# Kernel optimization log

Measured on AMD Instinct MI355X. Metric: run time of the kernel, lower is better.

The kernel has to match this reference:

```python
import jax, jax.numpy as jnp
import numpy as np

N, R, E, H, F = 50000, 6, 32768, 256, 16
NH, HD = 8, 32
EPS_LN = 1e-5

def _ln(x, g, b):
    mu = x.mean(-1, keepdims=True)
    var = ((x - mu) ** 2).mean(-1, keepdims=True)
    return (x - mu) * jax.lax.rsqrt(var + EPS_LN) * g + b

def setup_inputs() -> dict:
    key = jax.random.key(0)
    ks = jax.random.split(key, 32)
    s = lambda i, shape, scale=0.05: jax.random.normal(ks[i], shape, jnp.float32) * scale
    return {
        'x': jax.random.normal(ks[0], (N, H), jnp.float32),
        'edge_index': jax.random.randint(ks[1], (R, 2, E), 0, N, jnp.int32),
        'edge_attr': jax.random.normal(ks[2], (R, E, F), jnp.float32),
        'Wq': s(3, (R, H, H)), 'bq': s(4, (R, H)),
        'Wk': s(5, (R, H + F, H)), 'bk': s(6, (R, H)),
        'Wv': s(7, (R, H + F, H)), 'bv': s(8, (R, H)),
        'prior': jnp.ones((R, NH), jnp.float32),
        'Wm': s(9, (R, H, H)), 'bm': s(10, (R, H)),
        'W_ir1': s(11, (R * H, H)), 'b_ir1': s(12, (H,)),
        'W_ir2': s(13, (H, R)), 'b_ir2': s(14, (R,)),
        'Wmp': s(15, (3, H, H)), 'bmp': s(16, (3, H)),
        'Wa1': s(17, (H, H // 2)), 'ba1': s(18, (H // 2,)),
        'Wa2': s(19, (H // 2, 1)),
        'g_meta': jnp.ones((H,), jnp.float32), 'b_meta': jnp.zeros((H,), jnp.float32),
        'Wc': s(20, (2 * H, H)), 'bc': s(21, (H,)),
        'g_out': jnp.ones((H,), jnp.float32), 'b_out': jnp.zeros((H,), jnp.float32),
    }

def _block(x, edge_index, edge_attr, Wq, bq, Wk, bk, Wv, bv, prior, Wm, bm,
           W_ir1, b_ir1, W_ir2, b_ir2, Wmp, bmp, Wa1, ba1, Wa2, g_meta, b_meta,
           Wc, bc, g_out, b_out):
    def rel_layer(eidx, eattr, wq, bq_, wk, bk_, wv, bv_, pr, wm, bm_):
        src, dst = eidx[0], eidx[1]
        q = x @ wq + bq_                                  # [N,H]
        kv_in = jnp.concatenate([x[src], eattr], -1)      # [E,H+F]
        k = (kv_in @ wk + bk_).reshape(E, NH, HD)
        v = (kv_in @ wv + bv_).reshape(E, NH, HD)
        qe = q[dst].reshape(E, NH, HD)
        scores = (qe * k).sum(-1) / np.sqrt(HD) * pr      # [E,NH]
        m = jax.ops.segment_max(scores, dst, num_segments=N)
        ex = jnp.exp(scores - m[dst])
        denom = jax.ops.segment_sum(ex, dst, num_segments=N)
        w = ex / (denom[dst] + 1e-16)
        wv_flat = (w[..., None] * v).reshape(E, H)
        agg = jax.ops.segment_sum(wv_flat, dst, num_segments=N)  # [N,H]
        return jax.nn.gelu(agg @ wm + bm_, approximate=False)

    rel_out = jax.vmap(rel_layer)(edge_index, edge_attr, Wq, bq, Wk, bk, Wv, bv,
                                  prior, Wm, bm)          # [R,N,H]

    all_rel = jnp.transpose(rel_out, (1, 0, 2)).reshape(N, R * H)
    h = jax.nn.gelu(all_rel @ W_ir1 + b_ir1, approximate=False)
    inter_w = jax.nn.softmax(h @ W_ir2 + b_ir2, axis=-1)  # [N,R]
    inter_agg = jnp.einsum('nr,rnh->nh', inter_w, rel_out)

    # meta-paths: 0=entangle(ENTANGLE=2,SWAP=3) 1=control(CONTROL=4,ROTATION=0) 2=local(PAULI=1,TEMPORAL=5)
    paths = jnp.stack([rel_out[2] + rel_out[3], rel_out[4] + rel_out[0],
                       rel_out[1] + rel_out[5]], axis=1)  # [N,3,H]
    stacked = jnp.einsum('nph,phk->npk', paths, Wmp) + bmp
    attn = jax.nn.softmax((jnp.tanh(stacked @ Wa1 + ba1) @ Wa2).squeeze(-1), axis=1)
    meta = _ln((attn[..., None] * stacked).sum(1), g_meta, b_meta)

    combined = jax.nn.gelu(jnp.concatenate([inter_agg, meta], -1) @ Wc + bc,
                           approximate=False)
    return _ln(x + combined, g_out, b_out)

def reference(x, edge_index, edge_attr, Wq, bq, Wk, bk, Wv, bv, prior, Wm, bm,
              W_ir1, b_ir1, W_ir2, b_ir2, Wmp, bmp, Wa1, ba1, Wa2, g_meta, b_meta,
              Wc, bc, g_out, b_out):
    return _block(x, edge_index, edge_attr, Wq, bq, Wk, bk, Wv, bv, prior, Wm, bm,
                  W_ir1, b_ir1, W_ir2, b_ir2, Wmp, bmp, Wa1, ba1, Wa2,
                  g_meta, b_meta, Wc, bc, g_out, b_out)
```

## Files before the change

kernel.cpp:

```cpp
#include <hip/hip_runtime.h>
#include <hip/hip_bf16.h>

typedef __hip_bfloat16 bf16;
typedef __attribute__((ext_vector_type(8))) short short8;
typedef __attribute__((ext_vector_type(4))) float f32x4;

#define NN 50000
#define RR 6
#define EE 32768
#define HH 256
#define FF 16
#define NHEAD 8
#define KVP 320

struct __align__(8) bf16x4 { bf16 v[4]; };

__device__ __forceinline__ float b2f(bf16 v) { return __bfloat162float(v); }
__device__ __forceinline__ bf16 f2b(float v) { return __float2bfloat16(v); }
__device__ __forceinline__ short f2s(float f) { bf16 b = f2b(f); return __builtin_bit_cast(short, b); }
__device__ __forceinline__ float s2f(short s) { return b2f(__builtin_bit_cast(bf16, s)); }
__device__ __forceinline__ float gelu_f(float x) { return 0.5f * x * (1.0f + erff(x * 0.7071067811865476f)); }
__device__ __forceinline__ unsigned fkey(float f) { unsigned u = __float_as_uint(f); return (u & 0x80000000u) ? ~u : (u | 0x80000000u); }
__device__ __forceinline__ float fdec(unsigned k) { unsigned u = (k & 0x80000000u) ? (k & 0x7fffffffu) : ~k; return __uint_as_float(u); }

__device__ __forceinline__ void gl2lds16(const void* g, void* l) {
  __builtin_amdgcn_global_load_lds(
      (const __attribute__((address_space(1))) unsigned int*)g,
      (__attribute__((address_space(3))) unsigned int*)l, 16, 0, 0);
}

__global__ void zero_k(uint4* __restrict__ p, int n16)
{
  const uint4 z = make_uint4(0u, 0u, 0u, 0u);
  for (int i = blockIdx.x * blockDim.x + threadIdx.x; i < n16; i += gridDim.x * blockDim.x)
    p[i] = z;
}

__global__ void cvt_k(const float* __restrict__ in, bf16* __restrict__ out, int n4)
{
  const int i = blockIdx.x * 256 + threadIdx.x;
  if (i >= n4) return;
  const float4 f = ((const float4*)in)[i];
  bf16x4 o; o.v[0] = f2b(f.x); o.v[1] = f2b(f.y); o.v[2] = f2b(f.z); o.v[3] = f2b(f.w);
  ((bf16x4*)out)[i] = o;
}

__global__ void tconv_k(const float* __restrict__ in, bf16* __restrict__ out,
                        int K, int NC, int Kp, long izs, long ozs)
{
  __shared__ float t[32][33];
  in  += (size_t)blockIdx.z * izs;
  out += (size_t)blockIdx.z * ozs;
  const int kb = blockIdx.x * 32, nb = blockIdx.y * 32;
  const int tx = threadIdx.x & 31, ty = threadIdx.x >> 5;
  for (int i = ty; i < 32; i += 8) {
    const int k = kb + i, n = nb + tx;
    t[i][tx] = (k < K && n < NC) ? in[(size_t)k * NC + n] : 0.f;
  }
  __syncthreads();
  for (int i = ty; i < 32; i += 8) {
    const int n = nb + i, k = kb + tx;
    if (n < NC && k < Kp) out[(size_t)n * Kp + k] = f2b(t[tx][i]);
  }
}

__global__ void bkv_k(const float* __restrict__ bk, const float* __restrict__ bv,
                      float* __restrict__ bkv)
{
  const int i = blockIdx.x * 256 + threadIdx.x;
  if (i >= RR * 512) return;
  const int r = i >> 9, c = i & 511;
  bkv[i] = (c < 256) ? bk[r * 256 + c] : bv[r * 256 + (c - 256)];
}

__global__ void copyslot_k(const bf16* __restrict__ tmp, bf16* __restrict__ slot)
{
  const int i = blockIdx.x * 256 + threadIdx.x;
  if (i >= NN * 32) return;
  const int n = i >> 5, c = (i & 31) * 8;
  *(short8*)(slot + (size_t)n * 1536 + c) = *(const short8*)(tmp + (size_t)n * 256 + c);
}

template<int ASRC, int ACT, int ZMODE, typename TO>
__global__ __launch_bounds__(256) void mm_k(
    const void* __restrict__ Av, const bf16* __restrict__ A2, int lda,
    const int* __restrict__ src, const float* __restrict__ eattr,
    const bf16* __restrict__ Bt, const float* __restrict__ bias,
    const float* __restrict__ wa2, TO* __restrict__ C, int ldc,
    float* __restrict__ logits, int M, int K, int z0)
{
  __shared__ short lA[128 * 64];
  __shared__ short lB[128 * 64];
  const int tid = threadIdx.x;
  const int w = tid >> 6, l = tid & 63;
  const int col0 = blockIdx.x << 7;
  const int row0 = blockIdx.y << 7;
  const bf16* Ab = (const bf16*)Av;
  const bf16* A2b = A2;
  const bf16* Btz = Bt;
  const float* biasz = bias;
  TO* Cz = C;
  float* lg = logits;
  if constexpr (ZMODE == 1) {
    const int slots3[3] = {2, 4, 1};
    Ab = (const bf16*)Av + slots3[blockIdx.z] * 256;
    lg = logits + (size_t)blockIdx.z * M;
  } else if constexpr (ZMODE == 3) {
    const int r1s[3] = {2, 4, 1}, r2s[3] = {3, 0, 5};
    const int z = blockIdx.z + z0;
    Ab  = (const bf16*)Av + (size_t)r1s[z] * 256;
    A2b = A2 + (size_t)r2s[z] * 256;
    Btz = Bt + (size_t)z * 256 * K;
    biasz = bias + z * 256;
    Cz = C + (size_t)blockIdx.z * (size_t)M * 256;
  }
  const int wm = (w >> 1) << 6, wn = (w & 1) << 6;
  const int lane15 = l & 15, kq = l >> 4;

  f32x4 acc[4][4] = {};

  for (int k0 = 0; k0 < K; k0 += 64) {
#pragma unroll
    for (int i = 0; i < 4; ++i) {
      const int idx = (w * 4 + i) * 64 + l;
      const int row = idx >> 3, cg = idx & 7;
      const int scg = cg ^ (row & 7);
      const int r = min(row0 + row, M - 1);
      const int kc = k0 + scg * 8;
      if constexpr (ASRC == 0) {
        gl2lds16(Ab + (size_t)r * lda + kc, &lA[idx * 8]);
      } else if constexpr (ASRC == 2) {
        const short8 u  = *(const short8*)(Ab + (size_t)r * lda + kc);
        const short8 v2 = *(const short8*)(A2b + (size_t)r * lda + kc);
        short8 s;
#pragma unroll
        for (int j = 0; j < 8; ++j) s[j] = f2s(s2f(u[j]) + s2f(v2[j]));
        *(short8*)&lA[idx * 8] = s;
      } else {
        short8 s;
        if (kc < HH) {
          s = *(const short8*)((const bf16*)Av + (size_t)src[r] * HH + kc);
        } else if (kc < HH + FF) {
          const float* p = eattr + (size_t)r * FF + (kc - HH);
          const float4 f0 = *(const float4*)p;
          const float4 f1 = *(const float4*)(p + 4);
          s[0] = f2s(f0.x); s[1] = f2s(f0.y); s[2] = f2s(f0.z); s[3] = f2s(f0.w);
          s[4] = f2s(f1.x); s[5] = f2s(f1.y); s[6] = f2s(f1.z); s[7] = f2s(f1.w);
        } else {
#pragma unroll
          for (int j = 0; j < 8; ++j) s[j] = 0;
        }
        *(short8*)&lA[idx * 8] = s;
      }
    }
#pragma unroll
    for (int i = 0; i < 4; ++i) {
      const int idx = (w * 4 + i) * 64 + l;
      const int row = idx >> 3, cg = idx & 7;
      const int scg = cg ^ (row & 7);
      gl2lds16(Btz + (size_t)(col0 + row) * K + k0 + scg * 8, &lB[idx * 8]);
    }
    __syncthreads();
#pragma unroll
    for (int kk = 0; kk < 64; kk += 32) {
      short8 af[4], bfr[4];
#pragma unroll
      for (int t = 0; t < 4; ++t) {
        const int ra = wm + t * 16 + lane15;
        const int ca = ((kk >> 3) + kq) ^ (ra & 7);
        af[t] = *(const short8*)&lA[ra * 64 + ca * 8];
        const int rb = wn + t * 16 + lane15;
        const int cb = ((kk >> 3) + kq) ^ (rb & 7);
        bfr[t] = *(const short8*)&lB[rb * 64 + cb * 8];
      }
#pragma unroll
      for (int ti = 0; ti < 4; ++ti)
#pragma unroll
        for (int tj = 0; tj < 4; ++tj)
          acc[ti][tj] = __builtin_amdgcn_mfma_f32_16x16x32_bf16(af[ti], bfr[tj], acc[ti][tj], 0, 0, 0);
    }
    __syncthreads();
  }

  if constexpr (ZMODE != 1) {
#pragma unroll
    for (int ti = 0; ti < 4; ++ti) {
#pragma unroll
      for (int reg = 0; reg < 4; ++reg) {
        const int row = row0 + wm + ti * 16 + kq * 4 + reg;
        if (row >= M) continue;
#pragma unroll
        for (int tj = 0; tj < 4; ++tj) {
          const int col = col0 + wn + tj * 16 + lane15;
          float v = acc[ti][tj][reg] + biasz[col];
          if constexpr (ACT == 1) v = gelu_f(v);
          if constexpr (sizeof(TO) == 2) Cz[(size_t)row * ldc + col] = (TO)f2b(v);
          else                           Cz[(size_t)row * ldc + col] = (TO)v;
        }
      }
    }
  } else {
#pragma unroll
    for (int ti = 0; ti < 4; ++ti) {
#pragma unroll
      for (int reg = 0; reg < 4; ++reg) {
        float part = 0.f;
#pragma unroll
        for (int tj = 0; tj < 4; ++tj) {
          const int col = col0 + wn + tj * 16 + lane15;
          part += tanhf(acc[ti][tj][reg] + biasz[col]) * wa2[col];
        }
#pragma unroll
        for (int off = 8; off > 0; off >>= 1) part += __shfl_xor(part, off, 64);
        const int row = row0 + wm + ti * 16 + kq * 4 + reg;
        if (lane15 == 0 && row < M) atomicAdd(&lg[row], part);
      }
    }
  }
}

__global__ void scores_k(const bf16* __restrict__ q, const bf16* __restrict__ kv,
                         const int* __restrict__ dst_idx, const float* __restrict__ prior_r,
                         float* __restrict__ scores, unsigned* __restrict__ mkey)
{
  const int e = blockIdx.x, t = threadIdx.x;
  const int dst = dst_idx[e];
  float p = b2f(q[(size_t)dst * 1536 + t]) * b2f(kv[(size_t)e * 512 + t]);
#pragma unroll
  for (int off = 16; off > 0; off >>= 1) p += __shfl_down(p, off, 32);
  const int h = t >> 5;
  if ((t & 31) == 0) {
    const float s = p * 0.1767766952966369f * prior_r[h];
    scores[e * NHEAD + h] = s;
    atomicMax(&mkey[dst * NHEAD + h], fkey(s));
  }
}

__global__ void expden_k(const float* __restrict__ scores, const int* __restrict__ dst_idx,
                         const unsigned* __restrict__ mkey, float* __restrict__ ex,
                         float* __restrict__ denom)
{
  const int idx = blockIdx.x * 256 + threadIdx.x;
  if (idx >= EE * NHEAD) return;
  const int e = idx >> 3, h = idx & 7;
  const int dst = dst_idx[e];
  const float m = fdec(mkey[dst * NHEAD + h]);
  const float v = expf(scores[idx] - m);
  ex[idx] = v;
  atomicAdd(&denom[dst * NHEAD + h], v);
}

__global__ void agg_k(const float* __restrict__ ex, const float* __restrict__ denom,
                      const bf16* __restrict__ kv, const int* __restrict__ dst_idx,
                      float* __restrict__ agg)
{
  const int e = blockIdx.x, t = threadIdx.x, h = t >> 5;
  const int dst = dst_idx[e];
  const float w = ex[e * NHEAD + h] / (denom[dst * NHEAD + h] + 1e-16f);
  atomicAdd(&agg[(size_t)dst * HH + t], w * b2f(kv[(size_t)e * 512 + 256 + t]));
}

__global__ void interw_k(const bf16* __restrict__ h, const float* __restrict__ W2,
                         const float* __restrict__ b2, float* __restrict__ interw)
{
  const int wv = threadIdx.x >> 6, ln = threadIdx.x & 63;
  const int n = blockIdx.x * 4 + wv;
  if (n >= NN) return;
  float a[6] = {0.f, 0.f, 0.f, 0.f, 0.f, 0.f};
#pragma unroll
  for (int kq = 0; kq < 4; ++kq) {
    const int k = ln + (kq << 6);
    const float hv = b2f(h[(size_t)n * HH + k]);
#pragma unroll
    for (int j = 0; j < 6; ++j) a[j] += hv * W2[k * 6 + j];
  }
#pragma unroll
  for (int j = 0; j < 6; ++j) {
#pragma unroll
    for (int off = 32; off > 0; off >>= 1) a[j] += __shfl_down(a[j], off, 64);
  }
  if (ln == 0) {
    float lg[6], e[6], mx = -1e30f, s = 0.f;
#pragma unroll
    for (int j = 0; j < 6; ++j) { lg[j] = a[j] + b2[j]; mx = fmaxf(mx, lg[j]); }
#pragma unroll
    for (int j = 0; j < 6; ++j) { e[j] = expf(lg[j] - mx); s += e[j]; }
    const float inv = 1.0f / s;
#pragma unroll
    for (int j = 0; j < 6; ++j) interw[(size_t)n * 6 + j] = e[j] * inv;
  }
}

__global__ void interagg_k(const float* __restrict__ interw, const bf16* __restrict__ rel_cat,
                           bf16* __restrict__ comb)
{
  const int n = blockIdx.x, t = threadIdx.x;
  float acc = 0.f;
#pragma unroll
  for (int r = 0; r < 6; ++r)
    acc += interw[(size_t)n * 6 + r] * b2f(rel_cat[(size_t)n * 1536 + r * 256 + t]);
  comb[(size_t)n * 512 + t] = f2b(acc);
}

__global__ void metafinal_k(const float* __restrict__ logits, const bf16* __restrict__ rel_cat,
                            const float* __restrict__ gmeta, const float* __restrict__ bmeta,
                            bf16* __restrict__ comb)
{
  const int wv = threadIdx.x >> 6, ln = threadIdx.x & 63;
  const int n = blockIdx.x * 4 + wv;
  if (n >= NN) return;
  const float l0 = logits[n], l1 = logits[NN + n], l2 = logits[2 * NN + n];
  const float mx = fmaxf(l0, fmaxf(l1, l2));
  const float e0 = expf(l0 - mx), e1 = expf(l1 - mx), e2 = expf(l2 - mx);
  const float inv = 1.0f / (e0 + e1 + e2);
  const float a0 = e0 * inv, a1 = e1 * inv, a2 = e2 * inv;
  const size_t base = (size_t)n * 1536;
  float pre[4], s = 0.f, s2 = 0.f;
#pragma unroll
  for (int q4 = 0; q4 < 4; ++q4) {
    const int j = ln + (q4 << 6);
    const float v = a0 * b2f(rel_cat[base + 2 * 256 + j])
                  + a1 * b2f(rel_cat[base + 4 * 256 + j])
                  + a2 * b2f(rel_cat[base + 1 * 256 + j]);
    pre[q4] = v; s += v; s2 += v * v;
  }
#pragma unroll
  for (int off = 32; off > 0; off >>= 1) { s += __shfl_down(s, off, 64); s2 += __shfl_down(s2, off, 64); }
  s = __shfl(s, 0, 64); s2 = __shfl(s2, 0, 64);
  const float mu = s * (1.0f / 256.0f);
  const float var = s2 * (1.0f / 256.0f) - mu * mu;
  const float rs = rsqrtf(var + 1e-5f);
#pragma unroll
  for (int q4 = 0; q4 < 4; ++q4) {
    const int j = ln + (q4 << 6);
    comb[(size_t)n * 512 + 256 + j] = f2b((pre[q4] - mu) * rs * gmeta[j] + bmeta[j]);
  }
}

__global__ void final_k(const float* __restrict__ x, const float* __restrict__ combined,
                        const float* __restrict__ g, const float* __restrict__ b,
                        float* __restrict__ out)
{
  __shared__ float sred[8];
  const int n = blockIdx.x, t = threadIdx.x;
  const float v = x[(size_t)n * HH + t] + combined[(size_t)n * HH + t];
  float s = v, s2 = v * v;
#pragma unroll
  for (int off = 32; off > 0; off >>= 1) { s += __shfl_down(s, off, 64); s2 += __shfl_down(s2, off, 64); }
  const int wv = t >> 6;
  if ((t & 63) == 0) { sred[wv] = s; sred[4 + wv] = s2; }
  __syncthreads();
  const float st = sred[0] + sred[1] + sred[2] + sred[3];
  const float st2 = sred[4] + sred[5] + sred[6] + sred[7];
  const float mu = st * (1.0f / 256.0f);
  const float var = st2 * (1.0f / 256.0f) - mu * mu;
  const float rs = rsqrtf(var + 1e-5f);
  out[(size_t)n * HH + t] = (v - mu) * rs * g[t] + b[t];
}

extern "C" void kernel_launch(void* const* d_in, const int* in_sizes, int n_in,
                              void* d_out, int out_size, void* d_ws, size_t ws_size,
                              hipStream_t stream)
{
  const float* x      = (const float*)d_in[0];
  const int*   eidx   = (const int*)d_in[1];
  const float* eattr  = (const float*)d_in[2];
  const float* Wq     = (const float*)d_in[3];
  const float* bq     = (const float*)d_in[4];
  const float* Wk     = (const float*)d_in[5];
  const float* bk     = (const float*)d_in[6];
  const float* Wv     = (const float*)d_in[7];
  const float* bv     = (const float*)d_in[8];
  const float* prior  = (const float*)d_in[9];
  const float* Wm     = (const float*)d_in[10];
  const float* bm     = (const float*)d_in[11];
  const float* W_ir1  = (const float*)d_in[12];
  const float* b_ir1  = (const float*)d_in[13];
  const float* W_ir2  = (const float*)d_in[14];
  const float* b_ir2  = (const float*)d_in[15];
  const float* Wmp    = (const float*)d_in[16];
  const float* bmp    = (const float*)d_in[17];
  const float* Wa1    = (const float*)d_in[18];
  const float* ba1    = (const float*)d_in[19];
  const float* Wa2    = (const float*)d_in[20];
  const float* g_meta = (const float*)d_in[21];
  const float* b_meta = (const float*)d_in[22];
  const float* Wc     = (const float*)d_in[23];
  const float* bc     = (const float*)d_in[24];
  const float* g_out  = (const float*)d_in[25];
  const float* b_out  = (const float*)d_in[26];
  float* out = (float*)d_out;

  char* ws = (char*)d_ws;
  bf16* rel_cat = (bf16*)ws;
  char* W0 = ws + 153600000;
  bf16*  Wqt   = (bf16*)(W0 + 0);
  bf16*  Wkvt  = (bf16*)(W0 + 786432);
  bf16*  Wmt   = (bf16*)(W0 + 2752512);
  bf16*  Wir1t = (bf16*)(W0 + 3538944);
  bf16*  Wct   = (bf16*)(W0 + 4325376);
  bf16*  Wmpt  = (bf16*)(W0 + 4587520);
  bf16*  Wa1t  = (bf16*)(W0 + 4980736);
  float* bkv   = (float*)(W0 + 5046272);
  char* region = ws + 158658560;
  bf16*     kvbuf = (bf16*)(region + 0);
  float*    sc    = (float*)(region + 33554432);
  float*    exb   = (float*)(region + 34603008);
  unsigned* mkey  = (unsigned*)(region + 35651584);
  float*    denom = (float*)(region + 37251584);
  bf16*     xb    = (bf16*)(region + 38851584);
  float*    agg   = out;
  bf16*     aggb  = (bf16*)(region + 0);
  bf16*  hbuf     = (bf16*)(region + 0);
  float* interw   = (float*)(region + 33554432);
  bf16*  tmp      = (bf16*)(region + 0);
  float* logits   = (float*)(region + 51200000);
  bf16*  comb     = (bf16*)out;
  float* combined = (float*)(region + 0);

  const dim3 gN(2, 391);
  const dim3 gQ(12, 391);
  const dim3 gKV(4, 256);
  const dim3 gMP2(2, 391, 2);
  const dim3 gMP1(2, 391, 1);
  const dim3 gL(1, 391, 3);

  tconv_k<<<dim3(8, 8, 6), 256, 0, stream>>>(Wq, Wqt, 256, 256, 256, 256 * 256, 256 * 256);
  tconv_k<<<dim3(10, 8, 6), 256, 0, stream>>>(Wk, Wkvt, 272, 256, 320, 272 * 256, 512 * 320);
  tconv_k<<<dim3(10, 8, 6), 256, 0, stream>>>(Wv, Wkvt + 256 * 320, 272, 256, 320, 272 * 256, 512 * 320);
  tconv_k<<<dim3(8, 8, 6), 256, 0, stream>>>(Wm, Wmt, 256, 256, 256, 256 * 256, 256 * 256);
  tconv_k<<<dim3(48, 8, 1), 256, 0, stream>>>(W_ir1, Wir1t, 1536, 256, 1536, 0, 0);
  tconv_k<<<dim3(16, 8, 1), 256, 0, stream>>>(Wc, Wct, 512, 256, 512, 0, 0);
  tconv_k<<<dim3(8, 8, 3), 256, 0, stream>>>(Wmp, Wmpt, 256, 256, 256, 256 * 256, 256 * 256);
  tconv_k<<<dim3(8, 4, 1), 256, 0, stream>>>(Wa1, Wa1t, 256, 128, 256, 0, 0);
  bkv_k<<<12, 256, 0, stream>>>(bk, bv, bkv);
  cvt_k<<<(NN * 64 + 255) / 256, 256, 0, stream>>>(x, xb, NN * 64);

  mm_k<0, 0, 0, bf16><<<gQ, 256, 0, stream>>>(
      xb, nullptr, 256, nullptr, nullptr,
      Wqt, bq, nullptr, rel_cat, 1536, nullptr, NN, 256, 0);

  for (int r = 0; r < RR; ++r) {
    const int* src = eidx + (size_t)r * 2 * EE;
    const int* dst = src + EE;
    const float* ea = eattr + (size_t)r * EE * FF;
    zero_k<<<391, 256, 0, stream>>>((uint4*)mkey, (2 * NN * NHEAD * 4) / 16);
    zero_k<<<2048, 256, 0, stream>>>((uint4*)agg, (NN * HH * 4) / 16);
    mm_k<3, 0, 0, bf16><<<gKV, 256, 0, stream>>>(
        xb, nullptr, 0, src, ea,
        Wkvt + (size_t)r * 512 * KVP, bkv + r * 512, nullptr, kvbuf, 512, nullptr, EE, KVP, 0);
    scores_k<<<EE, 256, 0, stream>>>(rel_cat + r * 256, kvbuf, dst, prior + r * NHEAD, sc, mkey);
    expden_k<<<(EE * NHEAD + 255) / 256, 256, 0, stream>>>(sc, dst, mkey, exb, denom);
    agg_k<<<EE, 256, 0, stream>>>(exb, denom, kvbuf, dst, agg);
    cvt_k<<<(NN * 64 + 255) / 256, 256, 0, stream>>>(agg, (bf16*)aggb, NN * 64);
    mm_k<0, 1, 0, bf16><<<gN, 256, 0, stream>>>(
        aggb, nullptr, 256, nullptr, nullptr,
        Wmt + (size_t)r * 256 * 256, bm + r * HH, nullptr,
        rel_cat + r * 256, 1536, nullptr, NN, 256, 0);
  }

  mm_k<0, 1, 0, bf16><<<gN, 256, 0, stream>>>(
      rel_cat, nullptr, 1536, nullptr, nullptr,
      Wir1t, b_ir1, nullptr, hbuf, 256, nullptr, NN, 1536, 0);
  interw_k<<<(NN + 3) / 4, 256, 0, stream>>>(hbuf, W_ir2, b_ir2, interw);
  interagg_k<<<NN, 256, 0, stream>>>(interw, rel_cat, comb);

  mm_k<2, 0, 3, bf16><<<gMP2, 256, 0, stream>>>(
      rel_cat, rel_cat, 1536, nullptr, nullptr,
      Wmpt, bmp, nullptr, tmp, 256, nullptr, NN, 256, 0);
  copyslot_k<<<(NN * 32 + 255) / 256, 256, 0, stream>>>(tmp, rel_cat + 2 * 256);
  copyslot_k<<<(NN * 32 + 255) / 256, 256, 0, stream>>>(tmp + (size_t)NN * 256, rel_cat + 4 * 256);
  mm_k<2, 0, 3, bf16><<<gMP1, 256, 0, stream>>>(
      rel_cat, rel_cat, 1536, nullptr, nullptr,
      Wmpt, bmp, nullptr, tmp, 256, nullptr, NN, 256, 2);
  copyslot_k<<<(NN * 32 + 255) / 256, 256, 0, stream>>>(tmp, rel_cat + 1 * 256);

  zero_k<<<147, 256, 0, stream>>>((uint4*)logits, (3 * NN * 4) / 16);
  mm_k<0, 0, 1, bf16><<<gL, 256, 0, stream>>>(
      rel_cat, nullptr, 1536, nullptr, nullptr,
      Wa1t, ba1, Wa2, (bf16*)nullptr, 0, logits, NN, 256, 0);
  metafinal_k<<<(NN + 3) / 4, 256, 0, stream>>>(logits, rel_cat, g_meta, b_meta, comb);

  mm_k<0, 1, 0, float><<<gN, 256, 0, stream>>>(
      comb, nullptr, 512, nullptr, nullptr,
      Wct, bc, nullptr, combined, 256, nullptr, NN, 512, 0);
  final_k<<<NN, 256, 0, stream>>>(x, combined, g_out, b_out, out);
}
```

Before: 1.599 ms.

## Double-buffer GEMM LDS tiles, widen edge kernels, fuse fp32 agg conversion into GEMM

The GEMM kernel now double-buffers its A/B LDS tiles, prefetching the next K-tile while MFMAs run on the current one. Address math is hoisted out of the K loop. A new ASRC=1 path reads the fp32 aggregate directly, which removes the per-relation cvt_k pass. Edge attributes are pre-converted to bf16 once, and scores_k and agg_k now handle one edge per wavefront with 4-wide vector loads instead of one edge per 256-thread block. The cost is twice the LDS per block, which can lower occupancy, plus more register pressure from the prefetch buffers.

```diff
diff --git a/kernel.cpp b/kernel.cpp
--- a/kernel.cpp
+++ b/kernel.cpp
@@ -84,18 +84,19 @@
 template<int ASRC, int ACT, int ZMODE, typename TO>
 __global__ __launch_bounds__(256) void mm_k(
     const void* __restrict__ Av, const bf16* __restrict__ A2, int lda,
-    const int* __restrict__ src, const float* __restrict__ eattr,
+    const int* __restrict__ src, const bf16* __restrict__ eab,
     const bf16* __restrict__ Bt, const float* __restrict__ bias,
     const float* __restrict__ wa2, TO* __restrict__ C, int ldc,
     float* __restrict__ logits, int M, int K, int z0)
 {
-  __shared__ short lA[128 * 64];
-  __shared__ short lB[128 * 64];
+  __shared__ short lA[2][128 * 64];
+  __shared__ short lB[2][128 * 64];
   const int tid = threadIdx.x;
   const int w = tid >> 6, l = tid & 63;
   const int col0 = blockIdx.x << 7;
   const int row0 = blockIdx.y << 7;
   const bf16* Ab = (const bf16*)Av;
+  const float* Af = (const float*)Av;
   const bf16* A2b = A2;
   const bf16* Btz = Bt;
   const float* biasz = bias;
@@ -117,61 +118,100 @@
   const int wm = (w >> 1) << 6, wn = (w & 1) << 6;
   const int lane15 = l & 15, kq = l >> 4;
 
+  int idx8[4], rowi[4], scg8[4], ri[4], si[4];
+#pragma unroll
+  for (int i = 0; i < 4; ++i) {
+    const int idx = (w * 4 + i) * 64 + l;
+    rowi[i] = idx >> 3;
+    scg8[i] = ((idx & 7) ^ (rowi[i] & 7)) * 8;
+    idx8[i] = idx * 8;
+    ri[i]   = min(row0 + rowi[i], M - 1);
+    if constexpr (ASRC == 3) si[i] = src[ri[i]];
+  }
+
   f32x4 acc[4][4] = {};
-
-  for (int k0 = 0; k0 < K; k0 += 64) {
+  const int NT = K >> 6;
+
+  {
+    short8 ps[4], ps2[4]; float4 pf[8];
 #pragma unroll
     for (int i = 0; i < 4; ++i) {
-      const int idx = (w * 4 + i) * 64 + l;
-      const int row = idx >> 3, cg = idx & 7;
-      const int scg = cg ^ (row & 7);
-      const int r = min(row0 + row, M - 1);
-      const int kc = k0 + scg * 8;
+      const int kc = scg8[i];
+      gl2lds16(Btz + (size_t)(col0 + rowi[i]) * K + kc, &lB[0][idx8[i]]);
       if constexpr (ASRC == 0) {
-        gl2lds16(Ab + (size_t)r * lda + kc, &lA[idx * 8]);
+        gl2lds16(Ab + (size_t)ri[i] * lda + kc, &lA[0][idx8[i]]);
+      } else if constexpr (ASRC == 1) {
+        const float* p = Af + (size_t)ri[i] * lda + kc;
+        pf[2 * i] = *(const float4*)p; pf[2 * i + 1] = *(const float4*)(p + 4);
       } else if constexpr (ASRC == 2) {
-        const short8 u  = *(const short8*)(Ab + (size_t)r * lda + kc);
-        const short8 v2 = *(const short8*)(A2b + (size_t)r * lda + kc);
+        ps[i]  = *(const short8*)(Ab  + (size_t)ri[i] * lda + kc);
+        ps2[i] = *(const short8*)(A2b + (size_t)ri[i] * lda + kc);
+      } else {
+        if (kc < HH) ps[i] = *(const short8*)(Ab + (size_t)si[i] * HH + kc);
+        else if (kc < HH + FF) ps[i] = *(const short8*)(eab + (size_t)ri[i] * FF + (kc - HH));
+        else { short8 z; for (int j = 0; j < 8; ++j) z[j] = 0; ps[i] = z; }
+      }
+    }
+    if constexpr (ASRC == 1) {
+#pragma unroll
+      for (int i = 0; i < 4; ++i) {
         short8 s;
-#pragma unroll
-        for (int j = 0; j < 8; ++j) s[j] = f2s(s2f(u[j]) + s2f(v2[j]));
-        *(short8*)&lA[idx * 8] = s;
-      } else {
+        s[0] = f2s(pf[2*i].x); s[1] = f2s(pf[2*i].y); s[2] = f2s(pf[2*i].z); s[3] = f2s(pf[2*i].w);
+        s[4] = f2s(pf[2*i+1].x); s[5] = f2s(pf[2*i+1].y); s[6] = f2s(pf[2*i+1].z); s[7] = f2s(pf[2*i+1].w);
+        *(short8*)&lA[0][idx8[i]] = s;
+      }
+    } else if constexpr (ASRC == 2) {
+#pragma unroll
+      for (int i = 0; i < 4; ++i) {
         short8 s;
-        if (kc < HH) {
-          s = *(const short8*)((const bf16*)Av + (size_t)src[r] * HH + kc);
-        } else if (kc < HH + FF) {
-          const float* p = eattr + (size_t)r * FF + (kc - HH);
-          const float4 f0 = *(const float4*)p;
-          const float4 f1 = *(const float4*)(p + 4);
-          s[0] = f2s(f0.x); s[1] = f2s(f0.y); s[2] = f2s(f0.z); s[3] = f2s(f0.w);
-          s[4] = f2s(f1.x); s[5] = f2s(f1.y); s[6] = f2s(f1.z); s[7] = f2s(f1.w);
+#pragma unroll
+        for (int j = 0; j < 8; ++j) s[j] = f2s(s2f(ps[i][j]) + s2f(ps2[i][j]));
+        *(short8*)&lA[0][idx8[i]] = s;
+      }
+    } else if constexpr (ASRC == 3) {
+#pragma unroll
+      for (int i = 0; i < 4; ++i) *(short8*)&lA[0][idx8[i]] = ps[i];
+    }
+  }
+  __syncthreads();
+
+  int cur = 0;
+  for (int t = 0; t < NT; ++t) {
+    const int nb = cur ^ 1;
+    const bool pfch = (t + 1 < NT);
+    short8 ps[4], ps2[4]; float4 pf[8];
+    if (pfch) {
+      const int k0n = (t + 1) << 6;
+#pragma unroll
+      for (int i = 0; i < 4; ++i) {
+        const int kc = k0n + scg8[i];
+        gl2lds16(Btz + (size_t)(col0 + rowi[i]) * K + kc, &lB[nb][idx8[i]]);
+        if constexpr (ASRC == 0) {
+          gl2lds16(Ab + (size_t)ri[i] * lda + kc, &lA[nb][idx8[i]]);
+        } else if constexpr (ASRC == 1) {
+          const float* p = Af + (size_t)ri[i] * lda + kc;
+          pf[2 * i] = *(const float4*)p; pf[2 * i + 1] = *(const float4*)(p + 4);
+        } else if constexpr (ASRC == 2) {
+          ps[i]  = *(const short8*)(Ab  + (size_t)ri[i] * lda + kc);
+          ps2[i] = *(const short8*)(A2b + (size_t)ri[i] * lda + kc);
         } else {
-#pragma unroll
-          for (int j = 0; j < 8; ++j) s[j] = 0;
+          if (kc < HH) ps[i] = *(const short8*)(Ab + (size_t)si[i] * HH + kc);
+          else if (kc < HH + FF) ps[i] = *(const short8*)(eab + (size_t)ri[i] * FF + (kc - HH));
+          else { short8 z; for (int j = 0; j < 8; ++j) z[j] = 0; ps[i] = z; }
         }
-        *(short8*)&lA[idx * 8] = s;
-      }
-    }
-#pragma unroll
-    for (int i = 0; i < 4; ++i) {
-      const int idx = (w * 4 + i) * 64 + l;
-      const int row = idx >> 3, cg = idx & 7;
-      const int scg = cg ^ (row & 7);
-      gl2lds16(Btz + (size_t)(col0 + row) * K + k0 + scg * 8, &lB[idx * 8]);
-    }
-    __syncthreads();
+      }
+    }
 #pragma unroll
     for (int kk = 0; kk < 64; kk += 32) {
       short8 af[4], bfr[4];
 #pragma unroll
-      for (int t = 0; t < 4; ++t) {
-        const int ra = wm + t * 16 + lane15;
+      for (int tt = 0; tt < 4; ++tt) {
+        const int ra = wm + tt * 16 + lane15;
         const int ca = ((kk >> 3) + kq) ^ (ra & 7);
-        af[t] = *(const short8*)&lA[ra * 64 + ca * 8];
-        const int rb = wn + t * 16 + lane15;
+        af[tt] = *(const short8*)&lA[cur][ra * 64 + ca * 8];
+        const int rb = wn + tt * 16 + lane15;
         const int cb = ((kk >> 3) + kq) ^ (rb & 7);
-        bfr[t] = *(const short8*)&lB[rb * 64 + cb * 8];
+        bfr[tt] = *(const short8*)&lB[cur][rb * 64 + cb * 8];
       }
 #pragma unroll
       for (int ti = 0; ti < 4; ++ti)
@@ -179,7 +219,30 @@
         for (int tj = 0; tj < 4; ++tj)
           acc[ti][tj] = __builtin_amdgcn_mfma_f32_16x16x32_bf16(af[ti], bfr[tj], acc[ti][tj], 0, 0, 0);
     }
+    if (pfch) {
+      if constexpr (ASRC == 1) {
+#pragma unroll
+        for (int i = 0; i < 4; ++i) {
+          short8 s;
+          s[0] = f2s(pf[2*i].x); s[1] = f2s(pf[2*i].y); s[2] = f2s(pf[2*i].z); s[3] = f2s(pf[2*i].w);
+          s[4] = f2s(pf[2*i+1].x); s[5] = f2s(pf[2*i+1].y); s[6] = f2s(pf[2*i+1].z); s[7] = f2s(pf[2*i+1].w);
+          *(short8*)&lA[nb][idx8[i]] = s;
+        }
+      } else if constexpr (ASRC == 2) {
+#pragma unroll
+        for (int i = 0; i < 4; ++i) {
+          short8 s;
+#pragma unroll
+          for (int j = 0; j < 8; ++j) s[j] = f2s(s2f(ps[i][j]) + s2f(ps2[i][j]));
+          *(short8*)&lA[nb][idx8[i]] = s;
+        }
+      } else if constexpr (ASRC == 3) {
+#pragma unroll
+        for (int i = 0; i < 4; ++i) *(short8*)&lA[nb][idx8[i]] = ps[i];
+      }
+    }
     __syncthreads();
+    cur = nb;
   }
 
   if constexpr (ZMODE != 1) {
@@ -223,13 +286,17 @@
                          const int* __restrict__ dst_idx, const float* __restrict__ prior_r,
                          float* __restrict__ scores, unsigned* __restrict__ mkey)
 {
-  const int e = blockIdx.x, t = threadIdx.x;
+  const int wv = threadIdx.x >> 6, l = threadIdx.x & 63;
+  const int e = blockIdx.x * 4 + wv;
   const int dst = dst_idx[e];
-  float p = b2f(q[(size_t)dst * 1536 + t]) * b2f(kv[(size_t)e * 512 + t]);
-#pragma unroll
-  for (int off = 16; off > 0; off >>= 1) p += __shfl_down(p, off, 32);
-  const int h = t >> 5;
-  if ((t & 31) == 0) {
+  const bf16x4 qv = *(const bf16x4*)(q  + (size_t)dst * 1536 + l * 4);
+  const bf16x4 kq = *(const bf16x4*)(kv + (size_t)e * 512 + l * 4);
+  float p = b2f(qv.v[0]) * b2f(kq.v[0]) + b2f(qv.v[1]) * b2f(kq.v[1])
+          + b2f(qv.v[2]) * b2f(kq.v[2]) + b2f(qv.v[3]) * b2f(kq.v[3]);
+#pragma unroll
+  for (int off = 4; off > 0; off >>= 1) p += __shfl_down(p, off, 8);
+  if ((l & 7) == 0) {
+    const int h = l >> 3;
     const float s = p * 0.1767766952966369f * prior_r[h];
     scores[e * NHEAD + h] = s;
     atomicMax(&mkey[dst * NHEAD + h], fkey(s));
@@ -254,10 +321,15 @@
                       const bf16* __restrict__ kv, const int* __restrict__ dst_idx,
                       float* __restrict__ agg)
 {
-  const int e = blockIdx.x, t = threadIdx.x, h = t >> 5;
+  const int wv = threadIdx.x >> 6, l = threadIdx.x & 63;
+  const int e = blockIdx.x * 4 + wv;
   const int dst = dst_idx[e];
+  const int h = l >> 3;
   const float w = ex[e * NHEAD + h] / (denom[dst * NHEAD + h] + 1e-16f);
-  atomicAdd(&agg[(size_t)dst * HH + t], w * b2f(kv[(size_t)e * 512 + 256 + t]));
+  const bf16x4 vv = *(const bf16x4*)(kv + (size_t)e * 512 + 256 + l * 4);
+  float* ap = agg + (size_t)dst * HH + l * 4;
+#pragma unroll
+  for (int j = 0; j < 4; ++j) atomicAdd(ap + j, w * b2f(vv.v[j]));
 }
 
 __global__ void interw_k(const bf16* __restrict__ h, const float* __restrict__ W2,
@@ -409,8 +481,8 @@
   unsigned* mkey  = (unsigned*)(region + 35651584);
   float*    denom = (float*)(region + 37251584);
   bf16*     xb    = (bf16*)(region + 38851584);
+  bf16*     eab   = (bf16*)(region + 64451584);
   float*    agg   = out;
-  bf16*     aggb  = (bf16*)(region + 0);
   bf16*  hbuf     = (bf16*)(region + 0);
   float* interw   = (float*)(region + 33554432);
   bf16*  tmp      = (bf16*)(region + 0);
@@ -435,6 +507,7 @@
   tconv_k<<<dim3(8, 4, 1), 256, 0, stream>>>(Wa1, Wa1t, 256, 128, 256, 0, 0);
   bkv_k<<<12, 256, 0, stream>>>(bk, bv, bkv);
   cvt_k<<<(NN * 64 + 255) / 256, 256, 0, stream>>>(x, xb, NN * 64);
+  cvt_k<<<(RR * EE * FF / 4 + 255) / 256, 256, 0, stream>>>(eattr, eab, RR * EE * FF / 4);
 
   mm_k<0, 0, 0, bf16><<<gQ, 256, 0, stream>>>(
       xb, nullptr, 256, nullptr, nullptr,
@@ -443,18 +516,16 @@
   for (int r = 0; r < RR; ++r) {
     const int* src = eidx + (size_t)r * 2 * EE;
     const int* dst = src + EE;
-    const float* ea = eattr + (size_t)r * EE * FF;
     zero_k<<<391, 256, 0, stream>>>((uint4*)mkey, (2 * NN * NHEAD * 4) / 16);
     zero_k<<<2048, 256, 0, stream>>>((uint4*)agg, (NN * HH * 4) / 16);
     mm_k<3, 0, 0, bf16><<<gKV, 256, 0, stream>>>(
-        xb, nullptr, 0, src, ea,
+        xb, nullptr, 0, src, eab + (size_t)r * EE * FF,
         Wkvt + (size_t)r * 512 * KVP, bkv + r * 512, nullptr, kvbuf, 512, nullptr, EE, KVP, 0);
-    scores_k<<<EE, 256, 0, stream>>>(rel_cat + r * 256, kvbuf, dst, prior + r * NHEAD, sc, mkey);
+    scores_k<<<EE / 4, 256, 0, stream>>>(rel_cat + r * 256, kvbuf, dst, prior + r * NHEAD, sc, mkey);
     expden_k<<<(EE * NHEAD + 255) / 256, 256, 0, stream>>>(sc, dst, mkey, exb, denom);
-    agg_k<<<EE, 256, 0, stream>>>(exb, denom, kvbuf, dst, agg);
-    cvt_k<<<(NN * 64 + 255) / 256, 256, 0, stream>>>(agg, (bf16*)aggb, NN * 64);
-    mm_k<0, 1, 0, bf16><<<gN, 256, 0, stream>>>(
-        aggb, nullptr, 256, nullptr, nullptr,
+    agg_k<<<EE / 4, 256, 0, stream>>>(exb, denom, kvbuf, dst, agg);
+    mm_k<1, 1, 0, bf16><<<gN, 256, 0, stream>>>(
+        agg, nullptr, 256, nullptr, nullptr,
         Wmt + (size_t)r * 256 * 256, bm + r * HH, nullptr,
         rel_cat + r * 256, 1536, nullptr, NN, 256, 0);
   }
```

Result: slower. 2.025 ms (+26.6%).
